# Kernel optimization log

Hardware: AMD Instinct MI355X
Metric: run time of the kernel (lower is better)

Reference implementation:

```python
import jax, jax.numpy as jnp
import numpy as np

D_MODEL = 1024
NUM_EXPERTS = 16
TOP_K = 2
CAPACITY_FACTOR = 1.25
SINKHORN_ITERS = 3
AUX_LOSS_WEIGHT = 0.01


def setup_inputs() -> dict:
    key = jax.random.key(0)
    ks = jax.random.split(key, 6)
    d, e, h = D_MODEL, NUM_EXPERTS, 4 * D_MODEL
    sd = 1.0 / np.sqrt(d)
    sh = 1.0 / np.sqrt(h)
    return {
        "x": jax.random.normal(ks[0], (4, 2048, d), dtype=jnp.float32),
        "W_router": jax.random.uniform(ks[1], (d, e), jnp.float32, -sd, sd),
        "W1": jax.random.uniform(ks[2], (e, d, h), jnp.float32, -sd, sd),
        "b1": jax.random.uniform(ks[3], (e, h), jnp.float32, -sd, sd),
        "W2": jax.random.uniform(ks[4], (e, h, d), jnp.float32, -sh, sh),
        "b2": jax.random.uniform(ks[5], (e, d), jnp.float32, -sh, sh),
    }


def _moe_forward(x, W_router, W1, b1, W2, b2):
    B, S, D = x.shape
    E, K = NUM_EXPERTS, TOP_K
    N = B * S
    capacity = max(int(N * CAPACITY_FACTOR / E), K)  # static python int

    xf = x.reshape(N, D)
    router_logits = xf @ W_router                      # [N, E]
    probs = jax.nn.softmax(router_logits, axis=-1)
    # Sinkhorn balancing (as in source: row-normalize, col-normalize, rescale)
    for _ in range(SINKHORN_ITERS):
        probs = probs / probs.sum(axis=-1, keepdims=True)
        probs = probs / probs.sum(axis=0, keepdims=True)
        probs = probs * (N / E)

    weights, indices = jax.lax.top_k(probs, K)         # [N, K]
    weights = weights / weights.sum(axis=-1, keepdims=True)

    # --- dispatch: sequential slot allocation in (t, k) order ---
    flat_e = indices.reshape(-1)                       # [N*K]
    onehot = (flat_e[:, None] == jnp.arange(E)[None, :]).astype(jnp.int32)  # [N*K, E]
    # position of each dispatch within its expert = count of earlier same-expert entries
    pos = (jnp.cumsum(onehot, axis=0) * onehot).sum(-1) - 1                  # [N*K]
    mask = pos < capacity                              # dispatch_mask flattened
    total_counts = onehot.sum(0)                       # [E]
    token_counts = jnp.minimum(total_counts, capacity)

    safe_pos = jnp.where(mask, pos, 0)
    flat_idx = jnp.where(mask, flat_e * capacity + safe_pos, E * capacity)
    x_rep = jnp.repeat(xf, K, axis=0)                  # [N*K, D], (t,k) order
    buf = jnp.zeros((E * capacity + 1, D), dtype=x.dtype)
    buf = buf.at[flat_idx].set(x_rep)
    expert_input = buf[: E * capacity].reshape(E, capacity, D)

    # --- per-expert MLP (exact GELU, as torch.nn.GELU default) ---
    h = jnp.einsum('ecd,edf->ecf', expert_input, W1) + b1[:, None, :]
    h = jax.nn.gelu(h, approximate=False)
    expert_output = jnp.einsum('ecf,efd->ecd', h, W2) + b2[:, None, :]  # [E, cap, D]

    # --- weighted gather-combine ---
    gathered = expert_output[flat_e, safe_pos]         # [N*K, D]
    w = (weights.reshape(-1) * mask.astype(weights.dtype))[:, None]
    y = (gathered * w).reshape(N, K, D).sum(axis=1).reshape(B, S, D)

    aux_loss = AUX_LOSS_WEIGHT * E * (
        probs.mean(axis=0) * (token_counts.astype(probs.dtype) / N)
    ).sum()
    return y, aux_loss


def reference(x, W_router, W1, b1, W2, b2):
    return _moe_forward(x, W_router, W1, b1, W2, b2)
```

## Files before the change

kernel.cpp:

```cpp
#include <hip/hip_runtime.h>
#include <hip/hip_bf16.h>
#include <math.h>

#define NTOK 8192
#define DM   1024
#define NE   16
#define HD   4096
#define CAP  640
#define NCHUNK 64

typedef float f32x4 __attribute__((ext_vector_type(4)));
typedef _Float16 f16x8 __attribute__((ext_vector_type(8)));
typedef _Float16 f16x4 __attribute__((ext_vector_type(4)));

__device__ __forceinline__ void gload16(const void* g, void* l) {
  __builtin_amdgcn_global_load_lds(
      (const __attribute__((address_space(1))) unsigned int*)g,
      (__attribute__((address_space(3))) unsigned int*)l, 16, 0, 0);
}

__device__ __forceinline__ float gelu_fast(float v) {
  float v2 = v * v;
  float z2n = v * fmaf(-0.07135481627f, v2, -1.595769122f);
  float e = __expf(z2n);
  return v / (1.0f + e);
}

__global__ __launch_bounds__(256) void k_router(const float* __restrict__ x,
                                                const float* __restrict__ Wr,
                                                float* __restrict__ probs,
                                                float* __restrict__ pout) {
  int wave = threadIdx.x >> 6, lane = threadIdx.x & 63;
  int tok = blockIdx.x * 4 + wave;
  const float* xr = x + (size_t)tok * DM;
  float acc[NE];
#pragma unroll
  for (int e = 0; e < NE; ++e) acc[e] = 0.f;
  for (int d = lane; d < DM; d += 64) {
    float xv = xr[d];
    const float* w = Wr + (size_t)d * NE;
#pragma unroll
    for (int e = 0; e < NE; ++e) acc[e] = fmaf(xv, w[e], acc[e]);
  }
#pragma unroll
  for (int off = 32; off >= 1; off >>= 1) {
#pragma unroll
    for (int e = 0; e < NE; ++e) acc[e] += __shfl_xor(acc[e], off, 64);
  }
  float m = acc[0];
#pragma unroll
  for (int e = 1; e < NE; ++e) m = fmaxf(m, acc[e]);
  float s = 0.f;
#pragma unroll
  for (int e = 0; e < NE; ++e) { acc[e] = expf(acc[e] - m); s += acc[e]; }
  float inv = 1.0f / s;
#pragma unroll
  for (int e = 0; e < NE; ++e) acc[e] *= inv;
  if (lane < NE) probs[(size_t)tok * NE + lane] = acc[lane];
  __shared__ float wsum[4][NE];
  if (lane == 0) {
#pragma unroll
    for (int e = 0; e < NE; ++e) wsum[wave][e] = acc[e];
  }
  __syncthreads();
  if (threadIdx.x < NE)
    pout[blockIdx.x * NE + threadIdx.x] =
        wsum[0][threadIdx.x] + wsum[1][threadIdx.x] + wsum[2][threadIdx.x] + wsum[3][threadIdx.x];
}

__global__ __launch_bounds__(256) void k_sink(float* __restrict__ probs,
                                              const float* __restrict__ pin,
                                              float* __restrict__ pout) {
  __shared__ float csinv[NE];
  int tid = threadIdx.x;
  if (tid < NE) {
    float s = 0.f;
#pragma unroll
    for (int b = 0; b < 32; ++b) s += pin[b * NE + tid];
    csinv[tid] = 512.0f / s;
  }
  __syncthreads();
  int tok = blockIdx.x * 256 + tid;
  float* row = probs + (size_t)tok * NE;
  float p[NE]; float rs = 0.f;
#pragma unroll
  for (int e = 0; e < NE; ++e) { p[e] = row[e] * csinv[e]; rs += p[e]; }
  float rinv = 1.0f / rs;
#pragma unroll
  for (int e = 0; e < NE; ++e) { p[e] *= rinv; row[e] = p[e]; }
#pragma unroll
  for (int off = 32; off >= 1; off >>= 1) {
#pragma unroll
    for (int e = 0; e < NE; ++e) p[e] += __shfl_xor(p[e], off, 64);
  }
  __shared__ float wsum[4][NE];
  int lane = tid & 63, wave = tid >> 6;
  if (lane == 0) {
#pragma unroll
    for (int e = 0; e < NE; ++e) wsum[wave][e] = p[e];
  }
  __syncthreads();
  if (tid < NE)
    pout[blockIdx.x * NE + tid] =
        wsum[0][tid] + wsum[1][tid] + wsum[2][tid] + wsum[3][tid];
}

__global__ __launch_bounds__(256) void k_sink3(const float* __restrict__ probs,
                                               const float* __restrict__ pin,
                                               int* __restrict__ eidx,
                                               float* __restrict__ ew) {
  __shared__ float csinv[NE];
  int tid = threadIdx.x;
  if (tid < NE) {
    float s = 0.f;
#pragma unroll
    for (int b = 0; b < 32; ++b) s += pin[b * NE + tid];
    csinv[tid] = 512.0f / s;
  }
  __syncthreads();
  int tok = blockIdx.x * 256 + tid;
  const float* row = probs + (size_t)tok * NE;
  float v0 = -1e30f, v1 = -1e30f; int e0 = 0, e1 = 0;
#pragma unroll
  for (int e = 0; e < NE; ++e) {
    float v = row[e] * csinv[e];
    if (v > v0) { v1 = v0; e1 = e0; v0 = v; e0 = e; }
    else if (v > v1) { v1 = v; e1 = e; }
  }
  float s = v0 + v1;
  eidx[tok * 2] = e0; eidx[tok * 2 + 1] = e1;
  ew[tok * 2] = v0 / s; ew[tok * 2 + 1] = v1 / s;
}

__global__ __launch_bounds__(256) void k_hist(const int* __restrict__ eidx,
                                              int* __restrict__ cnt) {
  __shared__ int h[NE];
  int tid = threadIdx.x, c = blockIdx.x;
  if (tid < NE) h[tid] = 0;
  __syncthreads();
  atomicAdd(&h[eidx[c * 256 + tid]], 1);
  __syncthreads();
  if (tid < NE) cnt[c * NE + tid] = h[tid];
}

__global__ __launch_bounds__(64) void k_prefix(const int* __restrict__ cnt,
                                               int* __restrict__ base,
                                               int* __restrict__ counts,
                                               float* __restrict__ aux) {
  __shared__ int tot[NE];
  int e = threadIdx.x;
  if (e < NE) {
    int run = 0;
    for (int c = 0; c < NCHUNK; ++c) {
      base[c * NE + e] = run;
      run += cnt[c * NE + e];
    }
    counts[e] = run;
    tot[e] = min(run, CAP);
  }
  __syncthreads();
  if (e == 0) {
    int s = 0;
#pragma unroll
    for (int i = 0; i < NE; ++i) s += tot[i];
    *aux = 0.01f * (float)s / (float)NTOK;
  }
}

__global__ __launch_bounds__(256) void k_assign(const int* __restrict__ eidx,
                                                const int* __restrict__ base,
                                                int* __restrict__ slot_tok,
                                                int* __restrict__ tok2slot) {
  __shared__ int wcnt[4][NE];
  __shared__ int cbase[NE];
  int tid = threadIdx.x, c = blockIdx.x, lane = tid & 63, wave = tid >> 6;
  int i = c * 256 + tid;
  int myE = eidx[i];
  if (tid < NE) cbase[tid] = base[c * NE + tid];
  int mypre = 0;
#pragma unroll
  for (int e = 0; e < NE; ++e) {
    unsigned long long m = __ballot(myE == e);
    if (myE == e) mypre = __popcll(m & ((1ull << lane) - 1ull));
    if (lane == 0) wcnt[wave][e] = __popcll(m);
  }
  __syncthreads();
  int pre = 0;
  for (int w = 0; w < wave; ++w) pre += wcnt[w][myE];
  int pos = cbase[myE] + pre + mypre;
  if (pos < CAP) {
    slot_tok[myE * CAP + pos] = i >> 1;
    tok2slot[i] = myE * CAP + pos;
  } else {
    tok2slot[i] = -1;
  }
}

__global__ __launch_bounds__(256) void k_gather(const float* __restrict__ x,
                                                const int* __restrict__ slot_tok,
                                                _Float16* __restrict__ xg) {
  int row = blockIdx.x;
  int tok = slot_tok[row];
  int t = threadIdx.x;
  f16x4 h;
  if (tok >= 0) {
    float4 v = *(const float4*)(x + (size_t)tok * DM + t * 4);
    h[0] = (_Float16)v.x; h[1] = (_Float16)v.y; h[2] = (_Float16)v.z; h[3] = (_Float16)v.w;
  } else {
    h[0] = (_Float16)0.f; h[1] = (_Float16)0.f; h[2] = (_Float16)0.f; h[3] = (_Float16)0.f;
  }
  *(f16x4*)(xg + (size_t)row * DM + t * 4) = h;
}

template<int ROWS>
__device__ __forceinline__ void stage_tileA(const _Float16* gbase, int ld, int k0,
                                            _Float16* lds, int w, int lane) {
  constexpr int PER = (ROWS * 8) / 256;
#pragma unroll
  for (int i = 0; i < PER; ++i) {
    int ci = (w * PER + i) * 64 + lane;
    int row = ci >> 3, c = ci & 7;
    int cs = c ^ (row & 7);
    gload16(gbase + (size_t)row * ld + k0 + cs * 8, lds + (w * PER + i) * 512);
  }
}

__device__ __forceinline__ void loadB8(const float* gb, int ld, int k0, int tid, float4* L) {
  int nq = tid & 31, kc = tid >> 5;
  const float* p = gb + (size_t)(k0 + kc * 8) * ld + nq * 4;
#pragma unroll
  for (int j = 0; j < 8; ++j) L[j] = *(const float4*)(p + (size_t)j * ld);
}

__device__ __forceinline__ void writeB(_Float16* Bs, int tid, const float4* L) {
  int nq = tid & 31, kc = tid >> 5;
#pragma unroll
  for (int i = 0; i < 4; ++i) {
    int n = nq * 4 + i;
    int pos = kc ^ ((n ^ (n >> 2)) & 7);
    f16x8 v;
#pragma unroll
    for (int j = 0; j < 8; ++j) {
      float f = (i == 0) ? L[j].x : (i == 1) ? L[j].y : (i == 2) ? L[j].z : L[j].w;
      v[j] = (_Float16)f;
    }
    *(f16x8*)(Bs + n * 64 + pos * 8) = v;
  }
}

__global__ __launch_bounds__(256) void k_gemm1(const _Float16* __restrict__ xg,
                                               const float* __restrict__ W1,
                                               const float* __restrict__ b1,
                                               _Float16* __restrict__ hbuf) {
  int bid = blockIdx.x;
  int logical = (bid & 7) * 320 + (bid >> 3);
  int my = logical % 5;
  int nx = (logical / 5) % 32;
  int e  = logical / 160;
  int m0 = my * 128, n0 = nx * 128;
  __shared__ _Float16 smem[2 * 128 * 64];
  _Float16* As = smem;
  _Float16* Bs = smem + 128 * 64;
  const _Float16* Ab = xg + ((size_t)e * CAP + m0) * DM;
  const float*    Bb = W1 + (size_t)e * DM * HD + n0;
  int tid = threadIdx.x, lane = tid & 63, w = tid >> 6;
  int wr = w >> 1, wc = w & 1;
  int lr = lane & 15, kg = lane >> 4;

  f32x4 zero = {0.f, 0.f, 0.f, 0.f};
  f32x4 acc[4][4];
#pragma unroll
  for (int m = 0; m < 4; ++m)
#pragma unroll
    for (int n = 0; n < 4; ++n) acc[m][n] = zero;

  float4 L[8];
  loadB8(Bb, HD, 0, tid, L);
  for (int t = 0; t < 16; ++t) {
    __syncthreads();
    stage_tileA<128>(Ab, DM, t * 64, As, w, lane);
    writeB(Bs, tid, L);
    __syncthreads();
    if (t + 1 < 16) loadB8(Bb, HD, (t + 1) * 64, tid, L);
#pragma unroll
    for (int ks = 0; ks < 2; ++ks) {
      f16x8 af[4], bf[4];
#pragma unroll
      for (int m = 0; m < 4; ++m) {
        int row = wr * 64 + m * 16 + lr;
        int cs = (ks * 4 + kg) ^ (row & 7);
        af[m] = *(const f16x8*)(As + row * 64 + cs * 8);
      }
#pragma unroll
      for (int n = 0; n < 4; ++n) {
        int row = wc * 64 + n * 16 + lr;
        int cs = (ks * 4 + kg) ^ ((row ^ (row >> 2)) & 7);
        bf[n] = *(const f16x8*)(Bs + row * 64 + cs * 8);
      }
#pragma unroll
      for (int m = 0; m < 4; ++m)
#pragma unroll
        for (int n = 0; n < 4; ++n)
          acc[m][n] = __builtin_amdgcn_mfma_f32_16x16x32_f16(af[m], bf[n], acc[m][n], 0, 0, 0);
    }
  }
  __syncthreads();
  _Float16* Cb = smem;
  int lq = lane >> 4;
#pragma unroll
  for (int n = 0; n < 4; ++n) {
    int col = wc * 64 + n * 16 + lr;
    float bias = b1[(size_t)e * HD + n0 + col];
#pragma unroll
    for (int m = 0; m < 4; ++m) {
#pragma unroll
      for (int r = 0; r < 4; ++r) {
        int row = wr * 64 + m * 16 + lq * 4 + r;
        float v = gelu_fast(acc[m][n][r] + bias);
        Cb[row * 128 + (col ^ (((row >> 2) & 3) << 4))] = (_Float16)v;
      }
    }
  }
  __syncthreads();
  int rr = tid >> 4;
  int c8 = (tid & 15) * 8;
#pragma unroll
  for (int p = 0; p < 8; ++p) {
    int row = p * 16 + rr;
    int colx = c8 ^ (((row >> 2) & 3) << 4);
    f16x8 v = *(const f16x8*)(Cb + row * 128 + colx);
    *(f16x8*)(hbuf + ((size_t)e * CAP + m0 + row) * HD + n0 + c8) = v;
  }
}

__global__ __launch_bounds__(256) void k_gemm2(const _Float16* __restrict__ hbuf,
                                               const float* __restrict__ W2,
                                               const float* __restrict__ b2,
                                               _Float16* __restrict__ P0,
                                               _Float16* __restrict__ P1) {
  int bid = blockIdx.x;
  int logical = (bid & 7) * 160 + (bid >> 3);
  int my = logical % 5;
  int nx = (logical / 5) % 8;
  int ks2 = (logical / 40) & 1;
  int e  = logical / 80;
  int m0 = my * 128, n0 = nx * 128, kbase = ks2 * 2048;
  __shared__ _Float16 smem[2 * 128 * 64];
  _Float16* As = smem;
  _Float16* Bs = smem + 128 * 64;
  const _Float16* Ab = hbuf + ((size_t)e * CAP + m0) * HD;
  const float*    Bb = W2 + (size_t)e * HD * DM + n0;
  int tid = threadIdx.x, lane = tid & 63, w = tid >> 6;
  int wr = w >> 1, wc = w & 1;
  int lr = lane & 15, kg = lane >> 4;

  f32x4 zero = {0.f, 0.f, 0.f, 0.f};
  f32x4 acc[4][4];
#pragma unroll
  for (int m = 0; m < 4; ++m)
#pragma unroll
    for (int n = 0; n < 4; ++n) acc[m][n] = zero;

  float4 L[8];
  loadB8(Bb, DM, kbase, tid, L);
  for (int t = 0; t < 32; ++t) {
    __syncthreads();
    stage_tileA<128>(Ab, HD, kbase + t * 64, As, w, lane);
    writeB(Bs, tid, L);
    __syncthreads();
    if (t + 1 < 32) loadB8(Bb, DM, kbase + (t + 1) * 64, tid, L);
#pragma unroll
    for (int ks = 0; ks < 2; ++ks) {
      f16x8 af[4], bf[4];
#pragma unroll
      for (int m = 0; m < 4; ++m) {
        int row = wr * 64 + m * 16 + lr;
        int cs = (ks * 4 + kg) ^ (row & 7);
        af[m] = *(const f16x8*)(As + row * 64 + cs * 8);
      }
#pragma unroll
      for (int n = 0; n < 4; ++n) {
        int row = wc * 64 + n * 16 + lr;
        int cs = (ks * 4 + kg) ^ ((row ^ (row >> 2)) & 7);
        bf[n] = *(const f16x8*)(Bs + row * 64 + cs * 8);
      }
#pragma unroll
      for (int m = 0; m < 4; ++m)
#pragma unroll
        for (int n = 0; n < 4; ++n)
          acc[m][n] = __builtin_amdgcn_mfma_f32_16x16x32_f16(af[m], bf[n], acc[m][n], 0, 0, 0);
    }
  }
  __syncthreads();
  _Float16* Cb = smem;
  _Float16* P = (ks2 == 0) ? P0 : P1;
  int lq = lane >> 4;
  float bias[4];
#pragma unroll
  for (int n = 0; n < 4; ++n)
    bias[n] = (ks2 == 0) ? b2[(size_t)e * DM + n0 + wc * 64 + n * 16 + lr] : 0.f;
#pragma unroll
  for (int m = 0; m < 4; ++m) {
#pragma unroll
    for (int n = 0; n < 4; ++n) {
#pragma unroll
      for (int r = 0; r < 4; ++r) {
        int row = wr * 64 + m * 16 + lq * 4 + r;
        int col = wc * 64 + n * 16 + lr;
        Cb[row * 128 + (col ^ (((row >> 2) & 3) << 4))] = (_Float16)(acc[m][n][r] + bias[n]);
      }
    }
  }
  __syncthreads();
  int rr = tid >> 4;
  int c8 = (tid & 15) * 8;
#pragma unroll
  for (int p = 0; p < 8; ++p) {
    int row = p * 16 + rr;
    int colx = c8 ^ (((row >> 2) & 3) << 4);
    f16x8 v = *(const f16x8*)(Cb + row * 128 + colx);
    *(f16x8*)(P + ((size_t)e * CAP + m0 + row) * DM + n0 + c8) = v;
  }
}

__global__ __launch_bounds__(256) void k_combine(const _Float16* __restrict__ P0,
                                                 const _Float16* __restrict__ P1,
                                                 const int* __restrict__ tok2slot,
                                                 const float* __restrict__ ew,
                                                 float* __restrict__ y) {
  int t = blockIdx.x;
  int d = threadIdx.x * 4;
  int i0 = tok2slot[t * 2], i1 = tok2slot[t * 2 + 1];
  float w0 = ew[t * 2], w1 = ew[t * 2 + 1];
  float a0 = 0.f, a1 = 0.f, a2 = 0.f, a3 = 0.f;
  if (i0 >= 0) {
    f16x4 oa = *(const f16x4*)(P0 + (size_t)i0 * DM + d);
    f16x4 ob = *(const f16x4*)(P1 + (size_t)i0 * DM + d);
    a0 += w0 * ((float)oa[0] + (float)ob[0]); a1 += w0 * ((float)oa[1] + (float)ob[1]);
    a2 += w0 * ((float)oa[2] + (float)ob[2]); a3 += w0 * ((float)oa[3] + (float)ob[3]);
  }
  if (i1 >= 0) {
    f16x4 oa = *(const f16x4*)(P0 + (size_t)i1 * DM + d);
    f16x4 ob = *(const f16x4*)(P1 + (size_t)i1 * DM + d);
    a0 += w1 * ((float)oa[0] + (float)ob[0]); a1 += w1 * ((float)oa[1] + (float)ob[1]);
    a2 += w1 * ((float)oa[2] + (float)ob[2]); a3 += w1 * ((float)oa[3] + (float)ob[3]);
  }
  float4 out = make_float4(a0, a1, a2, a3);
  *(float4*)(y + (size_t)t * DM + d) = out;
}

extern "C" void kernel_launch(void* const* d_in, const int* in_sizes, int n_in,
                              void* d_out, int out_size, void* d_ws, size_t ws_size,
                              hipStream_t stream) {
  const float* x  = (const float*)d_in[0];
  const float* Wr = (const float*)d_in[1];
  const float* W1 = (const float*)d_in[2];
  const float* b1 = (const float*)d_in[3];
  const float* W2 = (const float*)d_in[4];
  const float* b2 = (const float*)d_in[5];
  float* y = (float*)d_out;
  float* aux = y + (size_t)out_size - 1;

  char* ws = (char*)d_ws;
  float* probs    = (float*)ws; ws += (size_t)NTOK * NE * 4;
  float* C0       = (float*)ws; ws += 32 * NE * 4;
  float* C1       = (float*)ws; ws += 32 * NE * 4;
  int*   eidx     = (int*)ws;   ws += NTOK * 2 * 4;
  float* ew       = (float*)ws; ws += NTOK * 2 * 4;
  int*   slot_tok = (int*)ws;   ws += NE * CAP * 4;
  int*   tok2slot = (int*)ws;   ws += NTOK * 2 * 4;
  int*   counts   = (int*)ws;   ws += 256;
  int*   cnt      = (int*)ws;   ws += NCHUNK * NE * 4;
  int*   cbase    = (int*)ws;   ws += NCHUNK * NE * 4;
  _Float16* xg    = (_Float16*)ws; ws += (size_t)NE * CAP * DM * 2;
  _Float16* hbuf  = (_Float16*)ws; ws += (size_t)NE * CAP * HD * 2;
  _Float16* P1b   = (_Float16*)ws; ws += (size_t)NE * CAP * DM * 2;
  _Float16* P0b   = xg;

  hipMemsetAsync(slot_tok, 0xFF, (size_t)NE * CAP * 4, stream);

  k_router<<<NTOK / 4, 256, 0, stream>>>(x, Wr, probs, C0);
  k_sink<<<32, 256, 0, stream>>>(probs, C0, C1);
  k_sink<<<32, 256, 0, stream>>>(probs, C1, C0);
  k_sink3<<<32, 256, 0, stream>>>(probs, C0, eidx, ew);
  k_hist<<<NCHUNK, 256, 0, stream>>>(eidx, cnt);
  k_prefix<<<1, 64, 0, stream>>>(cnt, cbase, counts, aux);
  k_assign<<<NCHUNK, 256, 0, stream>>>(eidx, cbase, slot_tok, tok2slot);
  k_gather<<<NE * CAP, 256, 0, stream>>>(x, slot_tok, xg);

  k_gemm1<<<2560, 256, 0, stream>>>(xg, W1, b1, hbuf);
  k_gemm2<<<1280, 256, 0, stream>>>(hbuf, W2, b2, P0b, P1b);

  k_combine<<<NTOK, 256, 0, stream>>>(P0b, P1b, tok2slot, ew, y);
}
```

Measured before the change: 461.2 us.

## Double-buffer A tiles with async global-to-LDS loads in expert GEMMs

Replaces the two-syncthreads K loop in both expert GEMMs with a software pipeline. A is double-buffered in LDS and the next A tile and B registers are prefetched before the MFMA phase, using explicit vmcnt/lgkmcnt waits and raw barriers in place of full syncthreads. MFMA blocks are wrapped in s_setprio to favour matrix issue. The aim is to hide global load latency behind compute. It raises LDS use per block, which may cut occupancy, and relies on hand-counted vmcnt values being correct.

```diff
diff --git a/kernel.cpp b/kernel.cpp
--- a/kernel.cpp
+++ b/kernel.cpp
@@ -212,16 +212,15 @@
   *(f16x4*)(xg + (size_t)row * DM + t * 4) = h;
 }
 
-template<int ROWS>
-__device__ __forceinline__ void stage_tileA(const _Float16* gbase, int ld, int k0,
-                                            _Float16* lds, int w, int lane) {
-  constexpr int PER = (ROWS * 8) / 256;
-#pragma unroll
-  for (int i = 0; i < PER; ++i) {
-    int ci = (w * PER + i) * 64 + lane;
+
+__device__ __forceinline__ void stage_tileA128(const _Float16* gbase, int ld, int k0,
+                                               _Float16* lds, int w, int lane) {
+#pragma unroll
+  for (int i = 0; i < 4; ++i) {
+    int ci = (w * 4 + i) * 64 + lane;
     int row = ci >> 3, c = ci & 7;
     int cs = c ^ (row & 7);
-    gload16(gbase + (size_t)row * ld + k0 + cs * 8, lds + (w * PER + i) * 512);
+    gload16(gbase + (size_t)row * ld + k0 + cs * 8, lds + (w * 4 + i) * 512);
   }
 }
 
@@ -247,6 +246,58 @@
     *(f16x8*)(Bs + n * 64 + pos * 8) = v;
   }
 }
+
+#define MFMA_PHASE(Ac, Bs)                                                         \
+  _Pragma("unroll")                                                                \
+  for (int ks = 0; ks < 2; ++ks) {                                                 \
+    f16x8 af[4], bf[4];                                                            \
+    _Pragma("unroll")                                                              \
+    for (int m = 0; m < 4; ++m) {                                                  \
+      int row = wr * 64 + m * 16 + lr;                                             \
+      int cs = (ks * 4 + kg) ^ (row & 7);                                          \
+      af[m] = *(const f16x8*)((Ac) + row * 64 + cs * 8);                           \
+    }                                                                              \
+    _Pragma("unroll")                                                              \
+    for (int n = 0; n < 4; ++n) {                                                  \
+      int row = wc * 64 + n * 16 + lr;                                             \
+      int cs = (ks * 4 + kg) ^ ((row ^ (row >> 2)) & 7);                           \
+      bf[n] = *(const f16x8*)((Bs) + row * 64 + cs * 8);                           \
+    }                                                                              \
+    __builtin_amdgcn_s_setprio(1);                                                 \
+    _Pragma("unroll")                                                              \
+    for (int m = 0; m < 4; ++m)                                                    \
+      _Pragma("unroll")                                                            \
+      for (int n = 0; n < 4; ++n)                                                  \
+        acc[m][n] = __builtin_amdgcn_mfma_f32_16x16x32_f16(af[m], bf[n], acc[m][n], 0, 0, 0); \
+    __builtin_amdgcn_s_setprio(0);                                                 \
+  }
+
+#define ASYNC_K_LOOP(NT, AB, ALD, BB, BLD, KBASE)                                  \
+  {                                                                                \
+    stage_tileA128((AB), (ALD), (KBASE), As0, w, lane);                            \
+    loadB8((BB), (BLD), (KBASE), tid, L);                                          \
+    asm volatile("s_waitcnt vmcnt(0)" ::: "memory");                               \
+    __builtin_amdgcn_s_barrier();                                                  \
+    __builtin_amdgcn_sched_barrier(0);                                             \
+    for (int t = 0; t < (NT); ++t) {                                               \
+      const _Float16* Ac = (t & 1) ? As1 : As0;                                    \
+      _Float16* An = (t & 1) ? As0 : As1;                                          \
+      writeB(Bs, tid, L);                                                          \
+      if (t + 1 < (NT)) {                                                          \
+        stage_tileA128((AB), (ALD), (KBASE) + (t + 1) * 64, An, w, lane);          \
+        loadB8((BB), (BLD), (KBASE) + (t + 1) * 64, tid, L);                       \
+      }                                                                            \
+      asm volatile("s_waitcnt lgkmcnt(0)" ::: "memory");                           \
+      __builtin_amdgcn_s_barrier();                                                \
+      __builtin_amdgcn_sched_barrier(0);                                           \
+      MFMA_PHASE(Ac, Bs);                                                          \
+      __builtin_amdgcn_sched_barrier(0);                                           \
+      if (t + 1 < (NT)) { asm volatile("s_waitcnt vmcnt(8)" ::: "memory"); }       \
+      else              { asm volatile("s_waitcnt vmcnt(0)" ::: "memory"); }       \
+      __builtin_amdgcn_s_barrier();                                                \
+      __builtin_amdgcn_sched_barrier(0);                                           \
+    }                                                                              \
+  }
 
 __global__ __launch_bounds__(256) void k_gemm1(const _Float16* __restrict__ xg,
                                                const float* __restrict__ W1,
@@ -258,52 +309,25 @@
   int nx = (logical / 5) % 32;
   int e  = logical / 160;
   int m0 = my * 128, n0 = nx * 128;
-  __shared__ _Float16 smem[2 * 128 * 64];
-  _Float16* As = smem;
-  _Float16* Bs = smem + 128 * 64;
+  __shared__ _Float16 smem[3 * 128 * 64];
+  _Float16* As0 = smem;
+  _Float16* As1 = smem + 8192;
+  _Float16* Bs  = smem + 16384;
   const _Float16* Ab = xg + ((size_t)e * CAP + m0) * DM;
   const float*    Bb = W1 + (size_t)e * DM * HD + n0;
   int tid = threadIdx.x, lane = tid & 63, w = tid >> 6;
   int wr = w >> 1, wc = w & 1;
   int lr = lane & 15, kg = lane >> 4;
 
-  f32x4 zero = {0.f, 0.f, 0.f, 0.f};
   f32x4 acc[4][4];
 #pragma unroll
   for (int m = 0; m < 4; ++m)
 #pragma unroll
-    for (int n = 0; n < 4; ++n) acc[m][n] = zero;
+    for (int n = 0; n < 4; ++n) acc[m][n] = (f32x4){0.f, 0.f, 0.f, 0.f};
 
   float4 L[8];
-  loadB8(Bb, HD, 0, tid, L);
-  for (int t = 0; t < 16; ++t) {
-    __syncthreads();
-    stage_tileA<128>(Ab, DM, t * 64, As, w, lane);
-    writeB(Bs, tid, L);
-    __syncthreads();
-    if (t + 1 < 16) loadB8(Bb, HD, (t + 1) * 64, tid, L);
-#pragma unroll
-    for (int ks = 0; ks < 2; ++ks) {
-      f16x8 af[4], bf[4];
-#pragma unroll
-      for (int m = 0; m < 4; ++m) {
-        int row = wr * 64 + m * 16 + lr;
-        int cs = (ks * 4 + kg) ^ (row & 7);
-        af[m] = *(const f16x8*)(As + row * 64 + cs * 8);
-      }
-#pragma unroll
-      for (int n = 0; n < 4; ++n) {
-        int row = wc * 64 + n * 16 + lr;
-        int cs = (ks * 4 + kg) ^ ((row ^ (row >> 2)) & 7);
-        bf[n] = *(const f16x8*)(Bs + row * 64 + cs * 8);
-      }
-#pragma unroll
-      for (int m = 0; m < 4; ++m)
-#pragma unroll
-        for (int n = 0; n < 4; ++n)
-          acc[m][n] = __builtin_amdgcn_mfma_f32_16x16x32_f16(af[m], bf[n], acc[m][n], 0, 0, 0);
-    }
-  }
+  ASYNC_K_LOOP(16, Ab, DM, Bb, HD, 0);
+
   __syncthreads();
   _Float16* Cb = smem;
   int lq = lane >> 4;
@@ -345,52 +369,25 @@
   int ks2 = (logical / 40) & 1;
   int e  = logical / 80;
   int m0 = my * 128, n0 = nx * 128, kbase = ks2 * 2048;
-  __shared__ _Float16 smem[2 * 128 * 64];
-  _Float16* As = smem;
-  _Float16* Bs = smem + 128 * 64;
+  __shared__ _Float16 smem[3 * 128 * 64];
+  _Float16* As0 = smem;
+  _Float16* As1 = smem + 8192;
+  _Float16* Bs  = smem + 16384;
   const _Float16* Ab = hbuf + ((size_t)e * CAP + m0) * HD;
   const float*    Bb = W2 + (size_t)e * HD * DM + n0;
   int tid = threadIdx.x, lane = tid & 63, w = tid >> 6;
   int wr = w >> 1, wc = w & 1;
   int lr = lane & 15, kg = lane >> 4;
 
-  f32x4 zero = {0.f, 0.f, 0.f, 0.f};
   f32x4 acc[4][4];
 #pragma unroll
   for (int m = 0; m < 4; ++m)
 #pragma unroll
-    for (int n = 0; n < 4; ++n) acc[m][n] = zero;
+    for (int n = 0; n < 4; ++n) acc[m][n] = (f32x4){0.f, 0.f, 0.f, 0.f};
 
   float4 L[8];
-  loadB8(Bb, DM, kbase, tid, L);
-  for (int t = 0; t < 32; ++t) {
-    __syncthreads();
-    stage_tileA<128>(Ab, HD, kbase + t * 64, As, w, lane);
-    writeB(Bs, tid, L);
-    __syncthreads();
-    if (t + 1 < 32) loadB8(Bb, DM, kbase + (t + 1) * 64, tid, L);
-#pragma unroll
-    for (int ks = 0; ks < 2; ++ks) {
-      f16x8 af[4], bf[4];
-#pragma unroll
-      for (int m = 0; m < 4; ++m) {
-        int row = wr * 64 + m * 16 + lr;
-        int cs = (ks * 4 + kg) ^ (row & 7);
-        af[m] = *(const f16x8*)(As + row * 64 + cs * 8);
-      }
-#pragma unroll
-      for (int n = 0; n < 4; ++n) {
-        int row = wc * 64 + n * 16 + lr;
-        int cs = (ks * 4 + kg) ^ ((row ^ (row >> 2)) & 7);
-        bf[n] = *(const f16x8*)(Bs + row * 64 + cs * 8);
-      }
-#pragma unroll
-      for (int m = 0; m < 4; ++m)
-#pragma unroll
-        for (int n = 0; n < 4; ++n)
-          acc[m][n] = __builtin_amdgcn_mfma_f32_16x16x32_f16(af[m], bf[n], acc[m][n], 0, 0, 0);
-    }
-  }
+  ASYNC_K_LOOP(32, Ab, HD, Bb, DM, kbase);
+
   __syncthreads();
   _Float16* Cb = smem;
   _Float16* P = (ks2 == 0) ? P0 : P1;
```

Result: faster. 384.4 us (-16.7%).
